# Performance work log

Hardware: AMD Instinct MI355X
Metric: run time of the kernel (lower is better)

The kernel has to match this reference:

```python
import jax, jax.numpy as jnp
import numpy as np
from jax import lax

B, N, DDESC = 8, 256, 128
COST_KP = 1.0
COST_DESC = 1.0
BLOCK = 128  # row block for L1 cdist


def setup_inputs() -> dict:
    key = jax.random.key(0)
    k1, k2, k3, k4, k5 = jax.random.split(key, 5)
    W, H = 640, 480
    wh = jnp.array([W, H], jnp.float32)
    kp1 = jax.random.uniform(k1, (B, N, 2)) * wh          # pixel coords
    kp2 = jax.random.uniform(k2, (B, N, 2)) * wh
    desc1 = jax.random.normal(k3, (B, N, DDESC))
    desc2 = jax.random.normal(k4, (B, N, DDESC))
    theta = jax.random.uniform(k5, (1,)) * (2.0 * jnp.pi)
    return {
        "theta": theta,
        "my_feature": jnp.concatenate([kp1, desc1], -1),
        "my_tf_feature": jnp.concatenate([kp2, desc2], -1),
        "my_width": W,
        "my_height": H,
    }


def _fundamental_8point(p1, p2):
    """Normalized 8-point algorithm (cv2.FM_8POINT): p2^T F p1 = 0, F[2,2]=1."""
    def norm(p):
        m = p.mean(0)
        d = jnp.sqrt(((p - m) ** 2).sum(1)).mean()
        s = jnp.sqrt(2.0) / d
        T = jnp.array([[1.0, 0.0, 0.0], [0.0, 1.0, 0.0], [0.0, 0.0, 0.0]]) * s \
            + jnp.zeros((3, 3)).at[0, 2].set(-s * m[0]).at[1, 2].set(-s * m[1]).at[2, 2].set(1.0)
        return (p - m) * s, T
    x1, T1 = norm(p1)
    x2, T2 = norm(p2)
    u1, v1 = x1[:, 0], x1[:, 1]
    u2, v2 = x2[:, 0], x2[:, 1]
    A = jnp.stack([u2 * u1, u2 * v1, u2, v2 * u1, v2 * v1, v2, u1, v1, jnp.ones_like(u1)], 1)
    _, _, Vt = jnp.linalg.svd(A, full_matrices=False)      # Vt: [9,9]
    Fm = Vt[-1].reshape(3, 3)
    U, S, Vt2 = jnp.linalg.svd(Fm)
    Fm = (U * S.at[2].set(0.0)) @ Vt2                      # enforce rank 2
    Fm = T2.T @ Fm @ T1
    return Fm / Fm[2, 2]


def _cdist_l1(a, b):
    """torch.cdist(p=1) without materializing [M,M,D]; blocked over rows."""
    M, D = a.shape
    ab = a.reshape(M // BLOCK, BLOCK, D)
    rows = lax.map(lambda blk: jnp.abs(blk[:, None, :] - b[None, :, :]).sum(-1), ab)
    return rows.reshape(M, b.shape[0])


def _cost_matrix(theta, my_feature, my_tf_feature, W, H):
    my_kp = my_feature[..., :2]
    my_tf_kp = my_tf_feature[..., :2]
    my_desc = my_feature[..., 2:]
    my_tf_desc = my_tf_feature[..., 2:]

    c, s = jnp.cos(theta[0]), jnp.sin(theta[0])
    zero = jnp.zeros(())
    one = jnp.ones(())
    Tm = jnp.stack([
        jnp.stack([c, -s, zero, zero]),
        jnp.stack([s, c, zero, zero]),
        jnp.stack([zero, zero, one, zero]),
        jnp.stack([zero, zero, zero, one]),
    ])  # make_transformation_M(theta, 0, 0): z-rotation, no translation

    # homogeneous image-centered coords: [B, 4, N]
    all_kp = jnp.stack([
        my_kp[:, :, 0] - 0.5 * W,
        -my_kp[:, :, 1] + 0.5 * H,
        jnp.zeros_like(my_kp[:, :, 0]),
        jnp.ones_like(my_kp[:, :, 0]),
    ], 1)
    cal = jnp.round(jnp.einsum('ij,bjn->bin', Tm, all_kp))[:, :2, :]  # [B,2,N]
    g = cal.transpose(0, 2, 1)                                        # [B,N,2]
    o = jnp.stack([g[..., 0] + 0.5 * W, -g[..., 1] + 0.5 * H], -1)    # back to pixels

    pts1 = my_tf_kp.astype(jnp.int32).reshape(B * N, 2).astype(jnp.float32)
    pts2 = o.astype(jnp.int32).reshape(B * N, 2).astype(jnp.float32)
    F = _fundamental_8point(pts1, pts2)

    ones = jnp.ones((B * N, 1), jnp.float32)
    p1h = jnp.concatenate([pts1, ones], 1)
    p2h = jnp.concatenate([pts2, ones], 1)
    cost_kp = jnp.abs((p1h @ F.astype(jnp.float32)) @ p2h.T)          # [BN, BN]

    cost_desc = _cdist_l1(my_desc.reshape(B * N, -1), my_tf_desc.reshape(B * N, -1))
    C = COST_KP * cost_kp + COST_DESC * cost_desc
    return C.reshape(B, N, B * N)


def _hungarian_np(cost):
    """scipy.optimize.linear_sum_assignment (JV shortest augmenting path), numpy."""
    cost = np.asarray(cost, dtype=np.float64)
    n = cost.shape[0]
    u = np.zeros(n)
    v = np.zeros(n)
    path = np.full(n, -1, dtype=np.int64)
    col4row = np.full(n, -1, dtype=np.int64)
    row4col = np.full(n, -1, dtype=np.int64)
    for cur_row in range(n):
        shortest = np.full(n, np.inf)
        remaining = np.ones(n, dtype=bool)
        SR = []
        i = cur_row
        min_val = 0.0
        sink = -1
        while sink == -1:
            SR.append(i)
            idx = np.nonzero(remaining)[0]
            r = min_val + cost[i, idx] - u[i] - v[idx]
            better = r < shortest[idx]
            bidx = idx[better]
            shortest[bidx] = r[better]
            path[bidx] = i
            jpos = idx[np.argmin(shortest[idx])]
            min_val = shortest[jpos]
            remaining[jpos] = False
            if row4col[jpos] == -1:
                sink = jpos
            else:
                i = row4col[jpos]
        u[cur_row] += min_val
        for i2 in SR:
            if i2 != cur_row:
                u[i2] += min_val - shortest[col4row[i2]]
        scanned = ~remaining
        v[scanned] -= min_val - shortest[scanned]
        j = sink
        while True:
            i2 = path[j]
            row4col[j] = i2
            col4row[i2], j = j, col4row[i2]
            if i2 == cur_row:
                break
    return col4row


def reference(theta, my_feature, my_tf_feature, my_width, my_height):
    C = _cost_matrix(theta, my_feature, my_tf_feature, float(my_width), float(my_height))
    Cn = np.asarray(jax.device_get(C))
    # diagonal [N,N] blocks: C.split(num_kp, -1) -> c[i] in the torch code
    cols = np.stack([_hungarian_np(Cn[i, :, i * N:(i + 1) * N]) for i in range(B)])
    rows = np.tile(np.arange(N), (B, 1))
    matches = jnp.asarray(np.stack([rows, cols], 1), dtype=jnp.int32)  # [B,2,N]
    return C, matches
```

## Files before the change

### kernel.cpp

```cpp
#include <hip/hip_runtime.h>
#include <hip/hip_bf16.h>
#include <cfloat>
#include <math.h>

#define BB 8
#define NN 256
#define BN 2048
#define DD 128
#define FEAT 130

__global__ __launch_bounds__(256) void prep_kernel(
    const float* __restrict__ theta,
    const float* __restrict__ feat1,
    const float* __restrict__ feat2,
    const int* __restrict__ wp, const int* __restrict__ hp,
    float* __restrict__ pts1, float* __restrict__ pts2) {
  int i = blockIdx.x * 256 + threadIdx.x;
  if (i >= BN) return;
  double W = (double)wp[0], H = (double)hp[0];
  double th = (double)theta[0];
  double c = cos(th), s = sin(th);
  double kx = (double)feat1[(size_t)i * FEAT + 0];
  double ky = (double)feat1[(size_t)i * FEAT + 1];
  double x = kx - 0.5 * W;
  double y = -ky + 0.5 * H;
  double calx = rint(c * x - s * y);
  double caly = rint(s * x + c * y);
  double ox = calx + 0.5 * W;
  double oy = -caly + 0.5 * H;
  pts2[2 * i]     = (float)(int)ox;
  pts2[2 * i + 1] = (float)(int)oy;
  pts1[2 * i]     = (float)(int)feat2[(size_t)i * FEAT + 0];
  pts1[2 * i + 1] = (float)(int)feat2[(size_t)i * FEAT + 1];
}

__device__ inline double wred(double x) {
#pragma unroll
  for (int off = 32; off > 0; off >>= 1) x += __shfl_down(x, off, 64);
  return x;
}

#define JROT(P, Q) {                                                          \
  double app_ = __shfl(Bc[P], P);                                             \
  double aqq_ = __shfl(Bc[Q], Q);                                             \
  double apq_ = __shfl(Bc[P], Q);                                             \
  double c_, s_;                                                              \
  if (fabs(apq_) > 1e-300) {                                                  \
    double tau_ = (aqq_ - app_) / (2.0 * apq_);                               \
    double t_ = (tau_ >= 0.0 ? 1.0 : -1.0) / (fabs(tau_) + sqrt(1.0 + tau_ * tau_)); \
    c_ = 1.0 / sqrt(1.0 + t_ * t_);                                           \
    s_ = t_ * c_;                                                             \
  } else { c_ = 1.0; s_ = 0.0; }                                              \
  const int prt_ = (jln == P) ? Q : ((jln == Q) ? P : jln);                   \
  const bool isP_ = (jln == P), isQ_ = (jln == Q);                            \
  _Pragma("unroll")                                                           \
  for (int ii = 0; ii < 9; ++ii) {                                            \
    double ob_ = __shfl(Bc[ii], prt_);                                        \
    double ov_ = __shfl(Vc[ii], prt_);                                        \
    if (isP_) { Bc[ii] = c_ * Bc[ii] - s_ * ob_; Vc[ii] = c_ * Vc[ii] - s_ * ov_; } \
    if (isQ_) { Bc[ii] = s_ * ob_ + c_ * Bc[ii]; Vc[ii] = s_ * ov_ + c_ * Vc[ii]; } \
  }                                                                           \
  { double rp_ = Bc[P], rq_ = Bc[Q];                                          \
    Bc[P] = c_ * rp_ - s_ * rq_; Bc[Q] = s_ * rp_ + c_ * rq_; } }

#define ROT3(P, Q) {                                                          \
  double apq_ = A3[P][Q];                                                     \
  double c_, s_;                                                              \
  if (fabs(apq_) > 1e-300) {                                                  \
    double tau_ = (A3[Q][Q] - A3[P][P]) / (2.0 * apq_);                       \
    double t_ = (tau_ >= 0.0 ? 1.0 : -1.0) / (fabs(tau_) + sqrt(1.0 + tau_ * tau_)); \
    c_ = 1.0 / sqrt(1.0 + t_ * t_); s_ = t_ * c_;                             \
  } else { c_ = 1.0; s_ = 0.0; }                                              \
  _Pragma("unroll")                                                           \
  for (int ii = 0; ii < 3; ++ii) { double a_ = A3[ii][P], b_ = A3[ii][Q];     \
    A3[ii][P] = c_ * a_ - s_ * b_; A3[ii][Q] = s_ * a_ + c_ * b_; }           \
  _Pragma("unroll")                                                           \
  for (int ii = 0; ii < 3; ++ii) { double a_ = A3[P][ii], b_ = A3[Q][ii];     \
    A3[P][ii] = c_ * a_ - s_ * b_; A3[Q][ii] = s_ * a_ + c_ * b_; }           \
  _Pragma("unroll")                                                           \
  for (int ii = 0; ii < 3; ++ii) { double a_ = V3[ii][P], b_ = V3[ii][Q];     \
    V3[ii][P] = c_ * a_ - s_ * b_; V3[ii][Q] = s_ * a_ + c_ * b_; } }

__global__ __launch_bounds__(256) void fmat_kernel(
    const float* __restrict__ pts1f, const float* __restrict__ pts2f,
    double* __restrict__ Fout) {
  __shared__ double sred[6];
  __shared__ double sATA[45];
  __shared__ double sV[9][16];
  __shared__ double sEv[16];
  const int tid = threadIdx.x;
  const int lane = tid & 63;
  if (tid < 6) sred[tid] = 0.0;
  if (tid < 45) sATA[tid] = 0.0;
  __syncthreads();

  double sx1 = 0, sy1 = 0, sx2 = 0, sy2 = 0;
  for (int p = tid; p < BN; p += 256) {
    sx1 += (double)pts1f[2 * p];     sy1 += (double)pts1f[2 * p + 1];
    sx2 += (double)pts2f[2 * p];     sy2 += (double)pts2f[2 * p + 1];
  }
  sx1 = wred(sx1); sy1 = wred(sy1); sx2 = wred(sx2); sy2 = wred(sy2);
  if (lane == 0) {
    atomicAdd(&sred[0], sx1); atomicAdd(&sred[1], sy1);
    atomicAdd(&sred[2], sx2); atomicAdd(&sred[3], sy2);
  }
  __syncthreads();
  const double m1x = sred[0] * (1.0 / BN), m1y = sred[1] * (1.0 / BN);
  const double m2x = sred[2] * (1.0 / BN), m2y = sred[3] * (1.0 / BN);

  double d1 = 0, d2 = 0;
  for (int p = tid; p < BN; p += 256) {
    double ax = (double)pts1f[2 * p] - m1x, ay = (double)pts1f[2 * p + 1] - m1y;
    double bx = (double)pts2f[2 * p] - m2x, by = (double)pts2f[2 * p + 1] - m2y;
    d1 += sqrt(ax * ax + ay * ay);
    d2 += sqrt(bx * bx + by * by);
  }
  d1 = wred(d1); d2 = wred(d2);
  if (lane == 0) { atomicAdd(&sred[4], d1); atomicAdd(&sred[5], d2); }
  __syncthreads();
  const double s1 = sqrt(2.0) / (sred[4] * (1.0 / BN));
  const double s2 = sqrt(2.0) / (sred[5] * (1.0 / BN));

  double acc45[45];
#pragma unroll
  for (int e = 0; e < 45; ++e) acc45[e] = 0.0;
  for (int p = tid; p < BN; p += 256) {
    double u1 = ((double)pts1f[2 * p]     - m1x) * s1;
    double v1 = ((double)pts1f[2 * p + 1] - m1y) * s1;
    double u2 = ((double)pts2f[2 * p]     - m2x) * s2;
    double v2 = ((double)pts2f[2 * p + 1] - m2y) * s2;
    double r[9] = {u2 * u1, u2 * v1, u2, v2 * u1, v2 * v1, v2, u1, v1, 1.0};
#pragma unroll
    for (int a = 0; a < 9; ++a)
#pragma unroll
      for (int b = a; b < 9; ++b)
        acc45[9 * a - (a * (a - 1)) / 2 + (b - a)] += r[a] * r[b];
  }
#pragma unroll
  for (int e = 0; e < 45; ++e) {
    double vv = wred(acc45[e]);
    if (lane == 0) atomicAdd(&sATA[e], vv);
  }
  __syncthreads();

  if (tid < 64) {
    const int jln = tid;
    double Bc[9], Vc[9];
#pragma unroll
    for (int i2 = 0; i2 < 9; ++i2) {
      if (jln < 9) {
        int a = i2 < jln ? i2 : jln;
        int b = i2 < jln ? jln : i2;
        Bc[i2] = sATA[9 * a - (a * (a - 1)) / 2 + (b - a)];
      } else Bc[i2] = 0.0;
      Vc[i2] = (i2 == jln) ? 1.0 : 0.0;
    }
    for (int sw = 0; sw < 7; ++sw) {
      JROT(0,1) JROT(0,2) JROT(0,3) JROT(0,4) JROT(0,5) JROT(0,6) JROT(0,7) JROT(0,8)
      JROT(1,2) JROT(1,3) JROT(1,4) JROT(1,5) JROT(1,6) JROT(1,7) JROT(1,8)
      JROT(2,3) JROT(2,4) JROT(2,5) JROT(2,6) JROT(2,7) JROT(2,8)
      JROT(3,4) JROT(3,5) JROT(3,6) JROT(3,7) JROT(3,8)
      JROT(4,5) JROT(4,6) JROT(4,7) JROT(4,8)
      JROT(5,6) JROT(5,7) JROT(5,8)
      JROT(6,7) JROT(6,8)
      JROT(7,8)
    }
    double ev = 0.0;
#pragma unroll
    for (int i2 = 0; i2 < 9; ++i2) if (jln == i2) ev = Bc[i2];
    if (jln < 9) {
      sEv[jln] = ev;
#pragma unroll
      for (int i2 = 0; i2 < 9; ++i2) sV[i2][jln] = Vc[i2];
    }
  }
  __syncthreads();

  if (tid == 0) {
    int jm = 0; double be = sEv[0];
#pragma unroll
    for (int jj = 1; jj < 9; ++jj) if (sEv[jj] < be) { be = sEv[jj]; jm = jj; }
    double F0[9];
#pragma unroll
    for (int i2 = 0; i2 < 9; ++i2) F0[i2] = sV[i2][jm];
    double M00 = F0[0], M01 = F0[1], M02 = F0[2];
    double M10 = F0[3], M11 = F0[4], M12 = F0[5];
    double M20 = F0[6], M21 = F0[7], M22 = F0[8];
    double A3[3][3], V3[3][3];
    A3[0][0] = M00*M00 + M10*M10 + M20*M20;
    A3[0][1] = M00*M01 + M10*M11 + M20*M21;
    A3[0][2] = M00*M02 + M10*M12 + M20*M22;
    A3[1][1] = M01*M01 + M11*M11 + M21*M21;
    A3[1][2] = M01*M02 + M11*M12 + M21*M22;
    A3[2][2] = M02*M02 + M12*M12 + M22*M22;
    A3[1][0] = A3[0][1]; A3[2][0] = A3[0][2]; A3[2][1] = A3[1][2];
#pragma unroll
    for (int ii = 0; ii < 3; ++ii)
#pragma unroll
      for (int jj = 0; jj < 3; ++jj) V3[ii][jj] = (ii == jj) ? 1.0 : 0.0;
    for (int sw = 0; sw < 10; ++sw) { ROT3(0,1) ROT3(0,2) ROT3(1,2) }
    double w0 = A3[0][0], w1 = A3[1][1], w2 = A3[2][2];
    double vx, vy, vz;
    if (w0 <= w1 && w0 <= w2)      { vx = V3[0][0]; vy = V3[1][0]; vz = V3[2][0]; }
    else if (w1 <= w2)             { vx = V3[0][1]; vy = V3[1][1]; vz = V3[2][1]; }
    else                           { vx = V3[0][2]; vy = V3[1][2]; vz = V3[2][2]; }
    double Mv0 = M00 * vx + M01 * vy + M02 * vz;
    double Mv1 = M10 * vx + M11 * vy + M12 * vz;
    double Mv2 = M20 * vx + M21 * vy + M22 * vz;
    double F200 = M00 - Mv0 * vx, F201 = M01 - Mv0 * vy, F202 = M02 - Mv0 * vz;
    double F210 = M10 - Mv1 * vx, F211 = M11 - Mv1 * vy, F212 = M12 - Mv1 * vz;
    double F220 = M20 - Mv2 * vx, F221 = M21 - Mv2 * vy, F222 = M22 - Mv2 * vz;
    double R00 = s2 * F200, R01 = s2 * F201, R02 = s2 * F202;
    double R10 = s2 * F210, R11 = s2 * F211, R12 = s2 * F212;
    double R20 = -s2 * m2x * F200 - s2 * m2y * F210 + F220;
    double R21 = -s2 * m2x * F201 - s2 * m2y * F211 + F221;
    double R22 = -s2 * m2x * F202 - s2 * m2y * F212 + F222;
    double D00 = s1 * R00, D10 = s1 * R10, D20 = s1 * R20;
    double D01 = s1 * R01, D11 = s1 * R11, D21 = s1 * R21;
    double D02 = -s1 * m1x * R00 - s1 * m1y * R01 + R02;
    double D12 = -s1 * m1x * R10 - s1 * m1y * R11 + R12;
    double D22 = -s1 * m1x * R20 - s1 * m1y * R21 + R22;
    Fout[0] = D00 / D22; Fout[1] = D01 / D22; Fout[2] = D02 / D22;
    Fout[3] = D10 / D22; Fout[4] = D11 / D22; Fout[5] = D12 / D22;
    Fout[6] = D20 / D22; Fout[7] = D21 / D22; Fout[8] = D22 / D22;
  }
}

__global__ __launch_bounds__(256) void cost_kernel(
    const float* __restrict__ feat1,
    const float* __restrict__ feat2,
    const float* __restrict__ pts1,
    const float* __restrict__ pts2,
    const double* __restrict__ Fd,
    float* __restrict__ Cout) {
  __shared__ float D1[128][68];
  __shared__ float D2[128][68];
  __shared__ float a0s[64], a1s[64], a2s[64], p2xs[64], p2ys[64];
  const int tid = threadIdx.x;
  const int rowbase = blockIdx.y * 64;
  const int colbase = blockIdx.x * 64;
#pragma unroll
  for (int it = 0; it < 32; ++it) {
    int idx = it * 256 + tid;
    int r = idx >> 7, k = idx & 127;
    D1[k][r] = feat1[(size_t)(rowbase + r) * FEAT + 2 + k];
    D2[k][r] = feat2[(size_t)(colbase + r) * FEAT + 2 + k];
  }
  if (tid < 64) {
    float x1 = pts1[2 * (rowbase + tid)], y1 = pts1[2 * (rowbase + tid) + 1];
    a0s[tid] = (float)(Fd[0] * x1 + Fd[3] * y1 + Fd[6]);
    a1s[tid] = (float)(Fd[1] * x1 + Fd[4] * y1 + Fd[7]);
    a2s[tid] = (float)(Fd[2] * x1 + Fd[5] * y1 + Fd[8]);
    p2xs[tid] = pts2[2 * (colbase + tid)];
    p2ys[tid] = pts2[2 * (colbase + tid) + 1];
  }
  __syncthreads();
  const int tx = tid & 15, ty = tid >> 4;
  float acc[4][4] = {};
#pragma unroll 4
  for (int k = 0; k < 128; ++k) {
    float4 av = *(const float4*)&D1[k][ty * 4];
    float4 bv = *(const float4*)&D2[k][tx * 4];
    float ar[4] = {av.x, av.y, av.z, av.w};
    float br[4] = {bv.x, bv.y, bv.z, bv.w};
#pragma unroll
    for (int r = 0; r < 4; ++r)
#pragma unroll
      for (int c = 0; c < 4; ++c)
        acc[r][c] += fabsf(ar[r] - br[c]);
  }
#pragma unroll
  for (int r = 0; r < 4; ++r) {
    int row = rowbase + ty * 4 + r;
    float a0 = a0s[ty * 4 + r], a1 = a1s[ty * 4 + r], a2 = a2s[ty * 4 + r];
    float4 o;
    float* op = &o.x;
#pragma unroll
    for (int c = 0; c < 4; ++c) {
      float kp = fabsf(a0 * p2xs[tx * 4 + c] + a1 * p2ys[tx * 4 + c] + a2);
      op[c] = acc[r][c] + kp;
    }
    *(float4*)&Cout[(size_t)row * BN + colbase + tx * 4] = o;
  }
}

#define NROWS_C 152

__device__ __forceinline__ unsigned long long sortkey(double d) {
  long long b = __double_as_longlong(d);
  long long m = (b >> 63) | (long long)0x8000000000000000LL;
  return (unsigned long long)(b ^ m);
}
__device__ __forceinline__ double unsortkey(unsigned long long k) {
  unsigned long long m = ((long long)k < 0) ? 0x8000000000000000ULL
                                            : 0xFFFFFFFFFFFFFFFFULL;
  return __longlong_as_double((long long)(k ^ m));
}

template<int CTRL>
__device__ __forceinline__ unsigned long long dppmin(unsigned long long x) {
  int lo = (int)(unsigned)(x & 0xFFFFFFFFULL);
  int hi = (int)(unsigned)(x >> 32);
  int lo2 = __builtin_amdgcn_update_dpp(0, lo, CTRL, 0xF, 0xF, true);
  int hi2 = __builtin_amdgcn_update_dpp(0, hi, CTRL, 0xF, 0xF, true);
  unsigned long long y =
      ((unsigned long long)(unsigned)hi2 << 32) | (unsigned)lo2;
  return y < x ? y : x;
}

template<int CTRL>
__device__ __forceinline__ unsigned dppmin32(unsigned x) {
  int y = __builtin_amdgcn_update_dpp(0, (int)x, CTRL, 0xF, 0xF, true);
  unsigned u = (unsigned)y;
  return u < x ? u : x;
}

__device__ __forceinline__ double rl64(double x, int l) {
  long long bb = __double_as_longlong(x);
  int lo = __builtin_amdgcn_readlane((int)(bb & 0xFFFFFFFFLL), l);
  int hi = __builtin_amdgcn_readlane((int)(bb >> 32), l);
  return __longlong_as_double(((long long)hi << 32) | (unsigned)lo);
}

__device__ __forceinline__ unsigned long long rdpair(unsigned ghi, unsigned glo, int l) {
  return ((unsigned long long)(unsigned)__builtin_amdgcn_readlane((int)ghi, l) << 32)
       | (unsigned)__builtin_amdgcn_readlane((int)glo, l);
}

struct RPick { unsigned long long g; int wl; int li; };

__device__ __forceinline__ RPick reduce_pick(unsigned long long kl, int myli) {
  unsigned hi = (unsigned)(kl >> 32);
  unsigned h = dppmin32<0x121>(hi);
  h = dppmin32<0x122>(h);
  h = dppmin32<0x124>(h);
  h = dppmin32<0x128>(h);
  unsigned g0 = (unsigned)__builtin_amdgcn_readlane((int)h, 0);
  unsigned g1 = (unsigned)__builtin_amdgcn_readlane((int)h, 16);
  unsigned g2 = (unsigned)__builtin_amdgcn_readlane((int)h, 32);
  unsigned g3 = (unsigned)__builtin_amdgcn_readlane((int)h, 48);
  unsigned ga = g0 < g1 ? g0 : g1, gb = g2 < g3 ? g2 : g3;
  unsigned mh = ga < gb ? ga : gb;
  unsigned long long bal = __ballot(hi == mh);
  unsigned long long g; int wl;
  if (__builtin_popcountll(bal) == 1) {
    wl = (int)__builtin_ctzll(bal);
    g = rdpair((unsigned)(kl >> 32), (unsigned)kl, wl);
  } else {
    unsigned long long gg = dppmin<0x121>(kl);
    gg = dppmin<0x122>(gg); gg = dppmin<0x124>(gg); gg = dppmin<0x128>(gg);
    unsigned glo2 = (unsigned)gg, ghi2 = (unsigned)(gg >> 32);
    unsigned long long r0 = rdpair(ghi2, glo2, 0);
    unsigned long long r1 = rdpair(ghi2, glo2, 16);
    unsigned long long r2 = rdpair(ghi2, glo2, 32);
    unsigned long long r3 = rdpair(ghi2, glo2, 48);
    unsigned long long ra = r0 < r1 ? r0 : r1, rb = r2 < r3 ? r2 : r3;
    g = ra < rb ? ra : rb;
    bal = __ballot(kl == g);
    wl = (int)__builtin_ctzll(bal);
  }
  int li = __builtin_amdgcn_readlane(myli, wl);
  RPick r; r.g = g; r.wl = wl; r.li = li; return r;
}

#define UPD(K, CK, KK, PP) {                                           \
  double d_ = (base + (double)(CK)) - v##K;                            \
  unsigned long long nk_ = sortkey(d_);                                \
  bool a_ = ((rem >> (K)) & 1u) && (nk_ < (KK));                       \
  (KK) = a_ ? nk_ : (KK);                                              \
  (PP) = a_ ? i : (PP); }

#define ROWLOAD(I) ((I) < NROWS_C ? *(const float4*)&rcache[(I)][lane * 4]   \
                                  : *(const float4*)(Cb + (size_t)(I) * BN + lane * 4))

__global__ __launch_bounds__(64) void hungarian_kernel(
    const float* __restrict__ C, float* __restrict__ out_matches) {
  const int b = blockIdx.x;
  const int lane = threadIdx.x;
  __shared__ float rcache[NROWS_C][NN];
  __shared__ int c4r_lds[NN];
  __shared__ float u_s[NN];
  const float* Cb = C + (size_t)b * NN * BN + (size_t)b * NN;

  for (int t = lane; t < NROWS_C * (NN / 4); t += 64) {
    int r = t >> 6, q = t & 63;
    *(float4*)&rcache[r][q * 4] = *(const float4*)(Cb + (size_t)r * BN + q * 4);
  }
  for (int r = lane; r < NN; r += 64) c4r_lds[r] = -1;
  __syncthreads();

  for (int i = 0; i < NN; ++i) {
    float4 cr = ROWLOAD(i);
    float m01 = fminf(cr.x, cr.y), m23 = fminf(cr.z, cr.w);
    unsigned fb = __float_as_uint(fminf(m01, m23));
    fb = dppmin32<0x121>(fb); fb = dppmin32<0x122>(fb);
    fb = dppmin32<0x124>(fb); fb = dppmin32<0x128>(fb);
    unsigned g0 = (unsigned)__builtin_amdgcn_readlane((int)fb, 0);
    unsigned g1 = (unsigned)__builtin_amdgcn_readlane((int)fb, 16);
    unsigned g2 = (unsigned)__builtin_amdgcn_readlane((int)fb, 32);
    unsigned g3 = (unsigned)__builtin_amdgcn_readlane((int)fb, 48);
    unsigned ga = g0 < g1 ? g0 : g1, gb = g2 < g3 ? g2 : g3;
    unsigned gm = ga < gb ? ga : gb;
    if (lane == 0) u_s[i] = __uint_as_float(gm);
  }
  __syncthreads();

  double cm0 = DBL_MAX, cm1 = DBL_MAX, cm2 = DBL_MAX, cm3 = DBL_MAX;
  int am0 = 0, am1 = 0, am2 = 0, am3 = 0;
  for (int i = 0; i < NN; ++i) {
    float4 cr = ROWLOAD(i);
    double uu = (double)u_s[i];
    double s0 = (double)cr.x - uu; if (s0 < cm0) { cm0 = s0; am0 = i; }
    double s1 = (double)cr.y - uu; if (s1 < cm1) { cm1 = s1; am1 = i; }
    double s2 = (double)cr.z - uu; if (s2 < cm2) { cm2 = s2; am2 = i; }
    double s3 = (double)cr.w - uu; if (s3 < cm3) { cm3 = s3; am3 = i; }
  }
  double v0 = cm0, v1 = cm1, v2 = cm2, v3 = cm3;

  int r4c0, r4c1, r4c2, r4c3;
  { int old = atomicCAS(&c4r_lds[am0], -1, lane * 4 + 0); r4c0 = (old == -1) ? am0 : -1; }
  { int old = atomicCAS(&c4r_lds[am1], -1, lane * 4 + 1); r4c1 = (old == -1) ? am1 : -1; }
  { int old = atomicCAS(&c4r_lds[am2], -1, lane * 4 + 2); r4c2 = (old == -1) ? am2 : -1; }
  { int old = atomicCAS(&c4r_lds[am3], -1, lane * 4 + 3); r4c3 = (old == -1) ? am3 : -1; }
  __syncthreads();
  int c4r0 = c4r_lds[lane * 4 + 0];
  int c4r1 = c4r_lds[lane * 4 + 1];
  int c4r2 = c4r_lds[lane * 4 + 2];
  int c4r3 = c4r_lds[lane * 4 + 3];
  double u40 = (r4c0 >= 0) ? (double)u_s[r4c0] : 0.0;
  double u41 = (r4c1 >= 0) ? (double)u_s[r4c1] : 0.0;
  double u42 = (r4c2 >= 0) ? (double)u_s[r4c2] : 0.0;
  double u43 = (r4c3 >= 0) ? (double)u_s[r4c3] : 0.0;

  const unsigned long long KMAX = 0xFFFFFFFFFFFFFFFFULL;

  for (int cur = 0; cur < NN; ++cur) {
    {
      int sl = cur & 3, ow = cur >> 2;
      int myc = (sl == 0) ? c4r0 : (sl == 1) ? c4r1 : (sl == 2) ? c4r2 : c4r3;
      if (__builtin_amdgcn_readlane(myc, ow) >= 0) continue;
    }
    unsigned long long k0 = KMAX, k1 = KMAX, k2 = KMAX, k3 = KMAX;
    int p0 = -1, p1 = -1, p2 = -1, p3 = -1;
    double shp0 = 0, shp1 = 0, shp2 = 0, shp3 = 0;
    unsigned rem = 0xFu;
    double minval = 0.0;
    const double ucur0 = (double)u_s[cur];
    double ui = ucur0;
    int i = cur;
    int sink = -1;
    while (true) {
      float4 cr = ROWLOAD(i);
      double base = minval - ui;
      UPD(0, cr.x, k0, p0)
      UPD(1, cr.y, k1, p1)
      UPD(2, cr.z, k2, p2)
      UPD(3, cr.w, k3, p3)
      unsigned long long m01 = k0 < k1 ? k0 : k1;
      unsigned long long m23 = k2 < k3 ? k2 : k3;
      unsigned long long kl = m01 < m23 ? m01 : m23;
      int myli = (k0 == kl) ? 0 : (k1 == kl) ? 1 : (k2 == kl) ? 2 : 3;
      RPick rm = reduce_pick(kl, myli);
      minval = unsortkey(rm.g);
      int jpos = rm.wl * 4 + rm.li;
      int mr = (rm.li == 0) ? r4c0 : (rm.li == 1) ? r4c1
             : (rm.li == 2) ? r4c2 : r4c3;
      int rc = __builtin_amdgcn_readlane(mr, rm.wl);
      double mu = (rm.li == 0) ? u40 : (rm.li == 1) ? u41
                : (rm.li == 2) ? u42 : u43;
      if (lane == rm.wl) {
        if (rm.li == 0)      { k0 = KMAX; shp0 = minval; }
        else if (rm.li == 1) { k1 = KMAX; shp1 = minval; }
        else if (rm.li == 2) { k2 = KMAX; shp2 = minval; }
        else                 { k3 = KMAX; shp3 = minval; }
        rem &= ~(1u << rm.li);
      }
      if (rc < 0) { sink = jpos; break; }
      ui = rl64(mu, rm.wl);
      i = rc;
    }
    if (!(rem & 1u)) { double dl = minval - shp0; v0 -= dl; if (r4c0 >= 0) u40 += dl; }
    if (!(rem & 2u)) { double dl = minval - shp1; v1 -= dl; if (r4c1 >= 0) u41 += dl; }
    if (!(rem & 4u)) { double dl = minval - shp2; v2 -= dl; if (r4c2 >= 0) u42 += dl; }
    if (!(rem & 8u)) { double dl = minval - shp3; v3 -= dl; if (r4c3 >= 0) u43 += dl; }
    int j = sink;
    while (true) {
      int slot = j & 3, ow = j >> 2;
      int myp = (slot == 0) ? p0 : (slot == 1) ? p1 : (slot == 2) ? p2 : p3;
      int i2 = __builtin_amdgcn_readlane(myp, ow);
      int s2 = i2 & 3, ow2 = i2 >> 2;
      int myc = (s2 == 0) ? c4r0 : (s2 == 1) ? c4r1 : (s2 == 2) ? c4r2 : c4r3;
      int jn = __builtin_amdgcn_readlane(myc, ow2);
      double newu;
      if (i2 == cur) {
        newu = ucur0 + minval;
      } else {
        int slj = jn & 3, owj = jn >> 2;
        double myuj = (slj == 0) ? u40 : (slj == 1) ? u41
                    : (slj == 2) ? u42 : u43;
        newu = rl64(myuj, owj);
      }
      if (lane == ow) {
        if (slot == 0) { r4c0 = i2; u40 = newu; }
        else if (slot == 1) { r4c1 = i2; u41 = newu; }
        else if (slot == 2) { r4c2 = i2; u42 = newu; }
        else { r4c3 = i2; u43 = newu; }
      }
      if (lane == ow2) {
        if (s2 == 0) c4r0 = j; else if (s2 == 1) c4r1 = j;
        else if (s2 == 2) c4r2 = j; else c4r3 = j;
      }
      if (i2 == cur) break;
      j = jn;
    }
  }

  float4 ridx, cidx;
  ridx.x = (float)(lane * 4 + 0); ridx.y = (float)(lane * 4 + 1);
  ridx.z = (float)(lane * 4 + 2); ridx.w = (float)(lane * 4 + 3);
  cidx.x = (float)c4r0; cidx.y = (float)c4r1;
  cidx.z = (float)c4r2; cidx.w = (float)c4r3;
  *(float4*)&out_matches[b * 2 * NN + lane * 4] = ridx;
  *(float4*)&out_matches[b * 2 * NN + NN + lane * 4] = cidx;
}

extern "C" void kernel_launch(void* const* d_in, const int* in_sizes, int n_in,
                              void* d_out, int out_size, void* d_ws, size_t ws_size,
                              hipStream_t stream) {
  const float* theta = (const float*)d_in[0];
  const float* feat1 = (const float*)d_in[1];
  const float* feat2 = (const float*)d_in[2];
  const int* wp = (const int*)d_in[3];
  const int* hp = (const int*)d_in[4];
  float* out = (float*)d_out;

  float* pts1 = (float*)d_ws;
  float* pts2 = pts1 + 2 * BN;
  double* Fd = (double*)(pts2 + 2 * BN);

  prep_kernel<<<BN / 256, 256, 0, stream>>>(theta, feat1, feat2, wp, hp, pts1, pts2);
  fmat_kernel<<<1, 256, 0, stream>>>(pts1, pts2, Fd);
  dim3 grid(BN / 64, BN / 64);
  cost_kernel<<<grid, 256, 0, stream>>>(feat1, feat2, pts1, pts2, Fd, out);
  hungarian_kernel<<<BB, 64, 0, stream>>>(out, out + (size_t)BN * BN);
}
```

Before: 1.956 ms.

## Add auction-style augmenting row reduction before shortest-path Hungarian phase

Inserts an augmenting row reduction phase, as in the Jonker-Volgenant algorithm, between the column-reduction initialisation and the shortest-augmenting-path loop. For each free row it finds the best and second-best reduced costs, assigns the row and lowers the column price, and either follows the displaced row or queues it for a second pass. The phase is capped at a fixed operation budget. The aim is to leave fewer free rows for the expensive per-row Dijkstra search. Row duals move from float to double shared storage so the new phase can update them, which changes the numerical path and adds work that may not pay off.

Measured after the change: 2.064 ms. 1.06x slower.

```diff
diff --git a/kernel.cpp b/kernel.cpp
--- a/kernel.cpp
+++ b/kernel.cpp
@@ -285,6 +285,7 @@
 }
 
 #define NROWS_C 152
+#define ARR_BUDGET 1024
 
 __device__ __forceinline__ unsigned long long sortkey(double d) {
   long long b = __double_as_longlong(d);
@@ -373,13 +374,19 @@
 #define ROWLOAD(I) ((I) < NROWS_C ? *(const float4*)&rcache[(I)][lane * 4]   \
                                   : *(const float4*)(Cb + (size_t)(I) * BN + lane * 4))
 
+#define R4C_OF(LI) ((LI) == 0 ? r4c0 : (LI) == 1 ? r4c1 : (LI) == 2 ? r4c2 : r4c3)
+#define U4_OF(LI)  ((LI) == 0 ? u40  : (LI) == 1 ? u41  : (LI) == 2 ? u42  : u43)
+
 __global__ __launch_bounds__(64) void hungarian_kernel(
     const float* __restrict__ C, float* __restrict__ out_matches) {
   const int b = blockIdx.x;
   const int lane = threadIdx.x;
   __shared__ float rcache[NROWS_C][NN];
   __shared__ int c4r_lds[NN];
-  __shared__ float u_s[NN];
+  __shared__ double u_sd[NN];
+  __shared__ int flistA[NN];
+  __shared__ int flistB[NN];
+  __shared__ int nfc;
   const float* Cb = C + (size_t)b * NN * BN + (size_t)b * NN;
 
   for (int t = lane; t < NROWS_C * (NN / 4); t += 64) {
@@ -387,6 +394,7 @@
     *(float4*)&rcache[r][q * 4] = *(const float4*)(Cb + (size_t)r * BN + q * 4);
   }
   for (int r = lane; r < NN; r += 64) c4r_lds[r] = -1;
+  if (lane == 0) nfc = 0;
   __syncthreads();
 
   for (int i = 0; i < NN; ++i) {
@@ -401,7 +409,7 @@
     unsigned g3 = (unsigned)__builtin_amdgcn_readlane((int)fb, 48);
     unsigned ga = g0 < g1 ? g0 : g1, gb = g2 < g3 ? g2 : g3;
     unsigned gm = ga < gb ? ga : gb;
-    if (lane == 0) u_s[i] = __uint_as_float(gm);
+    if (lane == 0) u_sd[i] = (double)__uint_as_float(gm);
   }
   __syncthreads();
 
@@ -409,7 +417,7 @@
   int am0 = 0, am1 = 0, am2 = 0, am3 = 0;
   for (int i = 0; i < NN; ++i) {
     float4 cr = ROWLOAD(i);
-    double uu = (double)u_s[i];
+    double uu = u_sd[i];
     double s0 = (double)cr.x - uu; if (s0 < cm0) { cm0 = s0; am0 = i; }
     double s1 = (double)cr.y - uu; if (s1 < cm1) { cm1 = s1; am1 = i; }
     double s2 = (double)cr.z - uu; if (s2 < cm2) { cm2 = s2; am2 = i; }
@@ -427,12 +435,102 @@
   int c4r1 = c4r_lds[lane * 4 + 1];
   int c4r2 = c4r_lds[lane * 4 + 2];
   int c4r3 = c4r_lds[lane * 4 + 3];
-  double u40 = (r4c0 >= 0) ? (double)u_s[r4c0] : 0.0;
-  double u41 = (r4c1 >= 0) ? (double)u_s[r4c1] : 0.0;
-  double u42 = (r4c2 >= 0) ? (double)u_s[r4c2] : 0.0;
-  double u43 = (r4c3 >= 0) ? (double)u_s[r4c3] : 0.0;
+  double u40 = (r4c0 >= 0) ? u_sd[r4c0] : 0.0;
+  double u41 = (r4c1 >= 0) ? u_sd[r4c1] : 0.0;
+  double u42 = (r4c2 >= 0) ? u_sd[r4c2] : 0.0;
+  double u43 = (r4c3 >= 0) ? u_sd[r4c3] : 0.0;
+
+  for (int r = lane; r < NN; r += 64)
+    if (c4r_lds[r] < 0) { int p = atomicAdd(&nfc, 1); flistA[p] = r; }
+  __syncthreads();
+  int cnt_in = nfc;
 
   const unsigned long long KMAX = 0xFFFFFFFFFFFFFFFFULL;
+
+  {
+    int budget = ARR_BUDGET;
+    int* curl = flistA;
+    int* nextl = flistB;
+    for (int pass = 0; pass < 2 && budget > 0; ++pass) {
+      int outn = 0;
+      for (int k = 0; k < cnt_in && budget > 0; ++k) {
+        int i = curl[k];
+        bool chain = true;
+        while (chain) {
+          if (--budget < 0) { chain = false; break; }
+          double uii = u_sd[i];
+          float4 cr = ROWLOAD(i);
+          unsigned long long k0 = sortkey(((double)cr.x - uii) - v0);
+          unsigned long long k1 = sortkey(((double)cr.y - uii) - v1);
+          unsigned long long k2 = sortkey(((double)cr.z - uii) - v2);
+          unsigned long long k3 = sortkey(((double)cr.w - uii) - v3);
+          unsigned long long m01 = k0 < k1 ? k0 : k1;
+          unsigned long long m23 = k2 < k3 ? k2 : k3;
+          unsigned long long kl = m01 < m23 ? m01 : m23;
+          int myli = (k0 == kl) ? 0 : (k1 == kl) ? 1 : (k2 == kl) ? 2 : 3;
+          RPick a = reduce_pick(kl, myli);
+          unsigned long long q0 = k0, q1 = k1, q2 = k2, q3 = k3;
+          if (lane == a.wl) {
+            if (a.li == 0) q0 = KMAX; else if (a.li == 1) q1 = KMAX;
+            else if (a.li == 2) q2 = KMAX; else q3 = KMAX;
+          }
+          unsigned long long n01 = q0 < q1 ? q0 : q1;
+          unsigned long long n23 = q2 < q3 ? q2 : q3;
+          unsigned long long kl2 = n01 < n23 ? n01 : n23;
+          int myli2 = (q0 == kl2) ? 0 : (q1 == kl2) ? 1 : (q2 == kl2) ? 2 : 3;
+          RPick s2 = reduce_pick(kl2, myli2);
+          double umin = unsortkey(a.g), usub = unsortkey(s2.g);
+          bool strict = (a.g < s2.g);
+          int mr1 = R4C_OF(a.li);
+          int own1 = __builtin_amdgcn_readlane(mr1, a.wl);
+          int jsel, disp;
+          if (strict || own1 < 0) {
+            jsel = a.wl * 4 + a.li;
+            disp = own1;
+          } else {
+            jsel = s2.wl * 4 + s2.li;
+            int mr2 = R4C_OF(s2.li);
+            disp = __builtin_amdgcn_readlane(mr2, s2.wl);
+          }
+          if (strict && lane == a.wl) {
+            double dec = usub - umin;
+            if (a.li == 0) v0 -= dec; else if (a.li == 1) v1 -= dec;
+            else if (a.li == 2) v2 -= dec; else v3 -= dec;
+          }
+          double unew = uii + usub;
+          { int ow = jsel >> 2, sl = jsel & 3;
+            if (lane == ow) {
+              if (sl == 0)      { r4c0 = i; u40 = unew; }
+              else if (sl == 1) { r4c1 = i; u41 = unew; }
+              else if (sl == 2) { r4c2 = i; u42 = unew; }
+              else              { r4c3 = i; u43 = unew; }
+            } }
+          { int ow = i >> 2, sl = i & 3;
+            if (lane == ow) {
+              if (sl == 0) c4r0 = jsel; else if (sl == 1) c4r1 = jsel;
+              else if (sl == 2) c4r2 = jsel; else c4r3 = jsel;
+            } }
+          if (lane == 0) u_sd[i] = unew;
+          if (disp >= 0) {
+            int ow = disp >> 2, sl = disp & 3;
+            if (lane == ow) {
+              if (sl == 0) c4r0 = -1; else if (sl == 1) c4r1 = -1;
+              else if (sl == 2) c4r2 = -1; else c4r3 = -1;
+            }
+            if (strict) {
+              i = disp;
+            } else {
+              if (lane == 0) nextl[outn] = disp;
+              outn++;
+              chain = false;
+            }
+          } else chain = false;
+        }
+      }
+      int* tmp = curl; curl = nextl; nextl = tmp;
+      cnt_in = outn;
+    }
+  }
 
   for (int cur = 0; cur < NN; ++cur) {
     {
@@ -445,7 +543,7 @@
     double shp0 = 0, shp1 = 0, shp2 = 0, shp3 = 0;
     unsigned rem = 0xFu;
     double minval = 0.0;
-    const double ucur0 = (double)u_s[cur];
+    const double ucur0 = u_sd[cur];
     double ui = ucur0;
     int i = cur;
     int sink = -1;
@@ -463,11 +561,9 @@
       RPick rm = reduce_pick(kl, myli);
       minval = unsortkey(rm.g);
       int jpos = rm.wl * 4 + rm.li;
-      int mr = (rm.li == 0) ? r4c0 : (rm.li == 1) ? r4c1
-             : (rm.li == 2) ? r4c2 : r4c3;
+      int mr = R4C_OF(rm.li);
       int rc = __builtin_amdgcn_readlane(mr, rm.wl);
-      double mu = (rm.li == 0) ? u40 : (rm.li == 1) ? u41
-                : (rm.li == 2) ? u42 : u43;
+      double mu = U4_OF(rm.li);
       if (lane == rm.wl) {
         if (rm.li == 0)      { k0 = KMAX; shp0 = minval; }
         else if (rm.li == 1) { k1 = KMAX; shp1 = minval; }
```

## Refine Hungarian dual initialization with extra row/column reduction pass and faster wave reductions

Applied to the files above, without the earlier changes.

The Hungarian initialization now runs a second round of duals: after the row-min and column-min passes it recomputes the row potentials against the column duals, then recomputes the column duals and their argmin for the greedy assignment. Row duals are kept in double in shared memory. The aim is a better initial matching, so fewer augmenting-path searches are needed in the serial phase. Wave-wide min reductions also switch to DPP row-shift plus row_bcast steps ending in a single readlane instead of four readlanes. This adds two extra full passes over the 256 rows, and it may change which tie is picked for the matching.

Result: slower. 2.013 ms (+2.9%).

```diff
diff --git a/kernel.cpp b/kernel.cpp
--- a/kernel.cpp
+++ b/kernel.cpp
@@ -297,22 +297,41 @@
   return __longlong_as_double((long long)(k ^ m));
 }
 
-template<int CTRL>
-__device__ __forceinline__ unsigned long long dppmin(unsigned long long x) {
-  int lo = (int)(unsigned)(x & 0xFFFFFFFFULL);
-  int hi = (int)(unsigned)(x >> 32);
-  int lo2 = __builtin_amdgcn_update_dpp(0, lo, CTRL, 0xF, 0xF, true);
-  int hi2 = __builtin_amdgcn_update_dpp(0, hi, CTRL, 0xF, 0xF, true);
+template<int CTRL, int RM>
+__device__ __forceinline__ unsigned dppm32(unsigned x) {
+  int y = __builtin_amdgcn_update_dpp((int)x, (int)x, CTRL, RM, 0xF, false);
+  unsigned u = (unsigned)y;
+  return u < x ? u : x;
+}
+template<int CTRL, int RM>
+__device__ __forceinline__ unsigned long long dppm64(unsigned long long x) {
+  int lo = (int)(unsigned)x, hi = (int)(unsigned)(x >> 32);
+  int lo2 = __builtin_amdgcn_update_dpp(lo, lo, CTRL, RM, 0xF, false);
+  int hi2 = __builtin_amdgcn_update_dpp(hi, hi, CTRL, RM, 0xF, false);
   unsigned long long y =
       ((unsigned long long)(unsigned)hi2 << 32) | (unsigned)lo2;
   return y < x ? y : x;
 }
 
-template<int CTRL>
-__device__ __forceinline__ unsigned dppmin32(unsigned x) {
-  int y = __builtin_amdgcn_update_dpp(0, (int)x, CTRL, 0xF, 0xF, true);
-  unsigned u = (unsigned)y;
-  return u < x ? u : x;
+__device__ __forceinline__ unsigned wave_min_u32(unsigned x) {
+  unsigned h = dppm32<0x111, 0xF>(x);
+  h = dppm32<0x112, 0xF>(h);
+  h = dppm32<0x114, 0xF>(h);
+  h = dppm32<0x118, 0xF>(h);
+  h = dppm32<0x142, 0xA>(h);
+  h = dppm32<0x143, 0xC>(h);
+  return (unsigned)__builtin_amdgcn_readlane((int)h, 63);
+}
+__device__ __forceinline__ unsigned long long wave_min_u64(unsigned long long x) {
+  unsigned long long h = dppm64<0x111, 0xF>(x);
+  h = dppm64<0x112, 0xF>(h);
+  h = dppm64<0x114, 0xF>(h);
+  h = dppm64<0x118, 0xF>(h);
+  h = dppm64<0x142, 0xA>(h);
+  h = dppm64<0x143, 0xC>(h);
+  unsigned lo = (unsigned)__builtin_amdgcn_readlane((int)(unsigned)h, 63);
+  unsigned hi = (unsigned)__builtin_amdgcn_readlane((int)(unsigned)(h >> 32), 63);
+  return ((unsigned long long)hi << 32) | lo;
 }
 
 __device__ __forceinline__ double rl64(double x, int l) {
@@ -321,41 +340,32 @@
   int hi = __builtin_amdgcn_readlane((int)(bb >> 32), l);
   return __longlong_as_double(((long long)hi << 32) | (unsigned)lo);
 }
-
 __device__ __forceinline__ unsigned long long rdpair(unsigned ghi, unsigned glo, int l) {
   return ((unsigned long long)(unsigned)__builtin_amdgcn_readlane((int)ghi, l) << 32)
        | (unsigned)__builtin_amdgcn_readlane((int)glo, l);
 }
 
+__device__ __forceinline__ unsigned long long reduce_key(unsigned long long kl) {
+  unsigned hi = (unsigned)(kl >> 32);
+  unsigned mh = wave_min_u32(hi);
+  unsigned long long bal = __ballot(hi == mh);
+  if (__builtin_popcountll(bal) == 1)
+    return rdpair(hi, (unsigned)kl, (int)__builtin_ctzll(bal));
+  return wave_min_u64(kl);
+}
+
 struct RPick { unsigned long long g; int wl; int li; };
 
 __device__ __forceinline__ RPick reduce_pick(unsigned long long kl, int myli) {
   unsigned hi = (unsigned)(kl >> 32);
-  unsigned h = dppmin32<0x121>(hi);
-  h = dppmin32<0x122>(h);
-  h = dppmin32<0x124>(h);
-  h = dppmin32<0x128>(h);
-  unsigned g0 = (unsigned)__builtin_amdgcn_readlane((int)h, 0);
-  unsigned g1 = (unsigned)__builtin_amdgcn_readlane((int)h, 16);
-  unsigned g2 = (unsigned)__builtin_amdgcn_readlane((int)h, 32);
-  unsigned g3 = (unsigned)__builtin_amdgcn_readlane((int)h, 48);
-  unsigned ga = g0 < g1 ? g0 : g1, gb = g2 < g3 ? g2 : g3;
-  unsigned mh = ga < gb ? ga : gb;
+  unsigned mh = wave_min_u32(hi);
   unsigned long long bal = __ballot(hi == mh);
   unsigned long long g; int wl;
   if (__builtin_popcountll(bal) == 1) {
     wl = (int)__builtin_ctzll(bal);
-    g = rdpair((unsigned)(kl >> 32), (unsigned)kl, wl);
+    g = rdpair(hi, (unsigned)kl, wl);
   } else {
-    unsigned long long gg = dppmin<0x121>(kl);
-    gg = dppmin<0x122>(gg); gg = dppmin<0x124>(gg); gg = dppmin<0x128>(gg);
-    unsigned glo2 = (unsigned)gg, ghi2 = (unsigned)(gg >> 32);
-    unsigned long long r0 = rdpair(ghi2, glo2, 0);
-    unsigned long long r1 = rdpair(ghi2, glo2, 16);
-    unsigned long long r2 = rdpair(ghi2, glo2, 32);
-    unsigned long long r3 = rdpair(ghi2, glo2, 48);
-    unsigned long long ra = r0 < r1 ? r0 : r1, rb = r2 < r3 ? r2 : r3;
-    g = ra < rb ? ra : rb;
+    g = wave_min_u64(kl);
     bal = __ballot(kl == g);
     wl = (int)__builtin_ctzll(bal);
   }
@@ -373,13 +383,16 @@
 #define ROWLOAD(I) ((I) < NROWS_C ? *(const float4*)&rcache[(I)][lane * 4]   \
                                   : *(const float4*)(Cb + (size_t)(I) * BN + lane * 4))
 
+#define R4C_OF(LI) ((LI) == 0 ? r4c0 : (LI) == 1 ? r4c1 : (LI) == 2 ? r4c2 : r4c3)
+#define U4_OF(LI)  ((LI) == 0 ? u40  : (LI) == 1 ? u41  : (LI) == 2 ? u42  : u43)
+
 __global__ __launch_bounds__(64) void hungarian_kernel(
     const float* __restrict__ C, float* __restrict__ out_matches) {
   const int b = blockIdx.x;
   const int lane = threadIdx.x;
   __shared__ float rcache[NROWS_C][NN];
   __shared__ int c4r_lds[NN];
-  __shared__ float u_s[NN];
+  __shared__ double u_sd[NN];
   const float* Cb = C + (size_t)b * NN * BN + (size_t)b * NN;
 
   for (int t = lane; t < NROWS_C * (NN / 4); t += 64) {
@@ -392,30 +405,50 @@
   for (int i = 0; i < NN; ++i) {
     float4 cr = ROWLOAD(i);
     float m01 = fminf(cr.x, cr.y), m23 = fminf(cr.z, cr.w);
-    unsigned fb = __float_as_uint(fminf(m01, m23));
-    fb = dppmin32<0x121>(fb); fb = dppmin32<0x122>(fb);
-    fb = dppmin32<0x124>(fb); fb = dppmin32<0x128>(fb);
-    unsigned g0 = (unsigned)__builtin_amdgcn_readlane((int)fb, 0);
-    unsigned g1 = (unsigned)__builtin_amdgcn_readlane((int)fb, 16);
-    unsigned g2 = (unsigned)__builtin_amdgcn_readlane((int)fb, 32);
-    unsigned g3 = (unsigned)__builtin_amdgcn_readlane((int)fb, 48);
-    unsigned ga = g0 < g1 ? g0 : g1, gb = g2 < g3 ? g2 : g3;
-    unsigned gm = ga < gb ? ga : gb;
-    if (lane == 0) u_s[i] = __uint_as_float(gm);
-  }
-  __syncthreads();
-
-  double cm0 = DBL_MAX, cm1 = DBL_MAX, cm2 = DBL_MAX, cm3 = DBL_MAX;
-  int am0 = 0, am1 = 0, am2 = 0, am3 = 0;
+    unsigned gm = wave_min_u32(__float_as_uint(fminf(m01, m23)));
+    if (lane == 0) u_sd[i] = (double)__uint_as_float(gm);
+  }
+  __syncthreads();
+
+  double v0, v1, v2, v3;
+  {
+    double c0 = DBL_MAX, c1 = DBL_MAX, c2 = DBL_MAX, c3 = DBL_MAX;
+    for (int i = 0; i < NN; ++i) {
+      float4 cr = ROWLOAD(i);
+      double uu = u_sd[i];
+      double s0 = (double)cr.x - uu; c0 = s0 < c0 ? s0 : c0;
+      double s1 = (double)cr.y - uu; c1 = s1 < c1 ? s1 : c1;
+      double s2 = (double)cr.z - uu; c2 = s2 < c2 ? s2 : c2;
+      double s3 = (double)cr.w - uu; c3 = s3 < c3 ? s3 : c3;
+    }
+    v0 = c0; v1 = c1; v2 = c2; v3 = c3;
+  }
+
+  __syncthreads();
   for (int i = 0; i < NN; ++i) {
     float4 cr = ROWLOAD(i);
-    double uu = (double)u_s[i];
-    double s0 = (double)cr.x - uu; if (s0 < cm0) { cm0 = s0; am0 = i; }
-    double s1 = (double)cr.y - uu; if (s1 < cm1) { cm1 = s1; am1 = i; }
-    double s2 = (double)cr.z - uu; if (s2 < cm2) { cm2 = s2; am2 = i; }
-    double s3 = (double)cr.w - uu; if (s3 < cm3) { cm3 = s3; am3 = i; }
-  }
-  double v0 = cm0, v1 = cm1, v2 = cm2, v3 = cm3;
+    double s0 = (double)cr.x - v0, s1 = (double)cr.y - v1;
+    double s2 = (double)cr.z - v2, s3 = (double)cr.w - v3;
+    double ma = s0 < s1 ? s0 : s1, mb = s2 < s3 ? s2 : s3;
+    unsigned long long kl = sortkey(ma < mb ? ma : mb);
+    unsigned long long g = reduce_key(kl);
+    if (lane == 0) u_sd[i] = unsortkey(g);
+  }
+  __syncthreads();
+
+  int am0 = 0, am1 = 0, am2 = 0, am3 = 0;
+  {
+    double c0 = DBL_MAX, c1 = DBL_MAX, c2 = DBL_MAX, c3 = DBL_MAX;
+    for (int i = 0; i < NN; ++i) {
+      float4 cr = ROWLOAD(i);
+      double uu = u_sd[i];
+      double s0 = (double)cr.x - uu; if (s0 < c0) { c0 = s0; am0 = i; }
+      double s1 = (double)cr.y - uu; if (s1 < c1) { c1 = s1; am1 = i; }
+      double s2 = (double)cr.z - uu; if (s2 < c2) { c2 = s2; am2 = i; }
+      double s3 = (double)cr.w - uu; if (s3 < c3) { c3 = s3; am3 = i; }
+    }
+    v0 = c0; v1 = c1; v2 = c2; v3 = c3;
+  }
 
   int r4c0, r4c1, r4c2, r4c3;
   { int old = atomicCAS(&c4r_lds[am0], -1, lane * 4 + 0); r4c0 = (old == -1) ? am0 : -1; }
@@ -427,10 +460,10 @@
   int c4r1 = c4r_lds[lane * 4 + 1];
   int c4r2 = c4r_lds[lane * 4 + 2];
   int c4r3 = c4r_lds[lane * 4 + 3];
-  double u40 = (r4c0 >= 0) ? (double)u_s[r4c0] : 0.0;
-  double u41 = (r4c1 >= 0) ? (double)u_s[r4c1] : 0.0;
-  double u42 = (r4c2 >= 0) ? (double)u_s[r4c2] : 0.0;
-  double u43 = (r4c3 >= 0) ? (double)u_s[r4c3] : 0.0;
+  double u40 = (r4c0 >= 0) ? u_sd[r4c0] : 0.0;
+  double u41 = (r4c1 >= 0) ? u_sd[r4c1] : 0.0;
+  double u42 = (r4c2 >= 0) ? u_sd[r4c2] : 0.0;
+  double u43 = (r4c3 >= 0) ? u_sd[r4c3] : 0.0;
 
   const unsigned long long KMAX = 0xFFFFFFFFFFFFFFFFULL;
 
@@ -445,7 +478,7 @@
     double shp0 = 0, shp1 = 0, shp2 = 0, shp3 = 0;
     unsigned rem = 0xFu;
     double minval = 0.0;
-    const double ucur0 = (double)u_s[cur];
+    const double ucur0 = u_sd[cur];
     double ui = ucur0;
     int i = cur;
     int sink = -1;
@@ -463,11 +496,9 @@
       RPick rm = reduce_pick(kl, myli);
       minval = unsortkey(rm.g);
       int jpos = rm.wl * 4 + rm.li;
-      int mr = (rm.li == 0) ? r4c0 : (rm.li == 1) ? r4c1
-             : (rm.li == 2) ? r4c2 : r4c3;
+      int mr = R4C_OF(rm.li);
       int rc = __builtin_amdgcn_readlane(mr, rm.wl);
-      double mu = (rm.li == 0) ? u40 : (rm.li == 1) ? u41
-                : (rm.li == 2) ? u42 : u43;
+      double mu = U4_OF(rm.li);
       if (lane == rm.wl) {
         if (rm.li == 0)      { k0 = KMAX; shp0 = minval; }
         else if (rm.li == 1) { k1 = KMAX; shp1 = minval; }
```
